# Kernel optimization log

Measured on AMD Instinct MI355X. Metric: run time of the kernel, lower is better.

## Reference

```python
import jax, jax.numpy as jnp
import numpy as np

B, T, I, H, O, L = 128, 512, 64, 256, 2, 2


def _gru_layer(x_seq, w_ih, w_hh, b_ih, b_hh):
    # x_seq: [B, T, in], w_ih: [3H, in], w_hh: [3H, H], biases: [3H]
    # PyTorch gate order: r, z, n
    xg = jnp.einsum('bti,gi->btg', x_seq, w_ih) + b_ih  # [B, T, 3H]
    h0 = jnp.zeros((x_seq.shape[0], w_hh.shape[1]), x_seq.dtype)

    def step(h, xg_t):
        hg = h @ w_hh.T + b_hh  # [B, 3H]
        xr, xz, xn = jnp.split(xg_t, 3, axis=-1)
        hr, hz, hn = jnp.split(hg, 3, axis=-1)
        r = jax.nn.sigmoid(xr + hr)
        z = jax.nn.sigmoid(xz + hz)
        n = jnp.tanh(xn + r * hn)
        h_new = (1.0 - z) * n + z * h
        return h_new, h_new

    _, hs = jax.lax.scan(step, h0, jnp.swapaxes(xg, 0, 1))  # [T, B, H]
    return jnp.swapaxes(hs, 0, 1)  # [B, T, H]


def setup_inputs() -> dict:
    key = jax.random.key(0)
    ks = jax.random.split(key, 12)
    s_ih0 = 1.0 / np.sqrt(H)
    inp = {
        'x': jax.random.normal(ks[0], (B, T, I), jnp.float32),
        'w_ih0': jax.random.uniform(ks[1], (3 * H, I), jnp.float32, -s_ih0, s_ih0),
        'w_hh0': jax.random.uniform(ks[2], (3 * H, H), jnp.float32, -s_ih0, s_ih0),
        'b_ih0': jax.random.uniform(ks[3], (3 * H,), jnp.float32, -s_ih0, s_ih0),
        'b_hh0': jax.random.uniform(ks[4], (3 * H,), jnp.float32, -s_ih0, s_ih0),
        'w_ih1': jax.random.uniform(ks[5], (3 * H, H), jnp.float32, -s_ih0, s_ih0),
        'w_hh1': jax.random.uniform(ks[6], (3 * H, H), jnp.float32, -s_ih0, s_ih0),
        'b_ih1': jax.random.uniform(ks[7], (3 * H,), jnp.float32, -s_ih0, s_ih0),
        'b_hh1': jax.random.uniform(ks[8], (3 * H,), jnp.float32, -s_ih0, s_ih0),
        'fc_w': jax.random.uniform(ks[9], (O, H), jnp.float32, -s_ih0, s_ih0),
        'fc_b': jax.random.uniform(ks[10], (O,), jnp.float32, -s_ih0, s_ih0),
    }
    return inp


def reference(x, w_ih0, w_hh0, b_ih0, b_hh0, w_ih1, w_hh1, b_ih1, b_hh1, fc_w, fc_b):
    h1 = _gru_layer(x, w_ih0, w_hh0, b_ih0, b_hh0)   # [B, T, H]
    h2 = _gru_layer(h1, w_ih1, w_hh1, b_ih1, b_hh1)  # [B, T, H]
    last = jax.nn.relu(h2[:, -1])                     # [B, H]
    return last @ fc_w.T + fc_b                       # [B, O]
```

## Files before the change

### kernel.cpp

```cpp
#include <hip/hip_runtime.h>


namespace {
constexpr int kB = 128, kT = 512, kI = 64, kH = 256, kBH = kB * kH;
constexpr int RPG = 16, NWG = 256, NT = 512;

constexpr int SRS = 36;
constexpr int SKS = 16 * SRS + 4;
constexpr int O_S0 = 0;
constexpr int O_S1 = O_S0 + 8 * SKS;
constexpr int O_X  = O_S1 + 8 * SKS;
constexpr int O_PB = O_X + RPG * 68;
constexpr int PBN  = 4 * 16 * 36;
constexpr int LDSF = O_PB + PBN;
}

using ull = unsigned long long;
using u32 = unsigned;

__device__ __forceinline__ float sigf(float v) { return 1.0f / (1.0f + expf(-v)); }
__device__ __forceinline__ float dot4(const float4 a, const float4 b) {
  return a.x * b.x + a.y * b.y + a.z * b.z + a.w * b.w;
}
__device__ __forceinline__ float red8(float v) {
  v += __shfl_xor(v, 8);
  v += __shfl_xor(v, 16);
  v += __shfl_xor(v, 32);
  return v;
}
#define F4(p) (*(const float4*)(p))
#define AL(p)    __hip_atomic_load((p), __ATOMIC_RELAXED, __HIP_MEMORY_SCOPE_AGENT)
#define AS(p, v) __hip_atomic_store((p), (v), __ATOMIC_RELAXED, __HIP_MEMORY_SCOPE_AGENT)

__global__ __launch_bounds__(NT, 2) void gru_persistent(
    const float* __restrict__ x,
    const float* __restrict__ wih0, const float* __restrict__ whh0,
    const float* __restrict__ bih0, const float* __restrict__ bhh0,
    const float* __restrict__ wih1, const float* __restrict__ whh1,
    const float* __restrict__ bih1, const float* __restrict__ bhh1,
    const float* __restrict__ fcw, const float* __restrict__ fcb,
    u32* __restrict__ h0w,
    u32* __restrict__ h1w,
    float* __restrict__ out)
{
  __shared__ float lds[2 * LDSF];

  const int bid = blockIdx.x;
  const int g   = bid >> 5;
  const int wg  = bid & 31;
  const int tid = threadIdx.x;
  const int r0  = g * RPG;
  const int j0  = wg * 8;

  const int wave = tid >> 6, lane = tid & 63;
  const int lay  = wave >> 2;
  const int fam  = (wave >> 1) & 1;
  const int rh   = wave & 1;
  const int ju   = lane & 7;
  const int ks   = lane >> 3;
  const int jg   = j0 + ju;

  for (int i = tid; i < PBN; i += NT) {
    lds[O_PB + i] = 0.f;
    lds[LDSF + O_PB + i] = 0.f;
  }

  float4 wr0[8], wr1[8], wr2[8];
  if (lay == 0) {
    if (fam == 0) {
#define L0F0(wrg, gg) { \
      const float* wi = wih0 + (size_t)((gg) * kH + jg) * kI + ks * 8;   \
      const float* wh = whh0 + (size_t)((gg) * kH + jg) * kH + ks * 32;  \
      wrg[0] = F4(wi); wrg[1] = F4(wi + 4);                              \
      wrg[2] = F4(wh); wrg[3] = F4(wh + 4); wrg[4] = F4(wh + 8); }
      L0F0(wr0, 0) L0F0(wr1, 1) L0F0(wr2, 2)
    } else {
#define L0F1(wrg, gg) { \
      const float* wh = whh0 + (size_t)((gg) * kH + jg) * kH + ks * 32 + 12; \
      wrg[0] = F4(wh); wrg[1] = F4(wh + 4); wrg[2] = F4(wh + 8);             \
      wrg[3] = F4(wh + 12); wrg[4] = F4(wh + 16); }
      L0F1(wr0, 0) L0F1(wr1, 1) L0F1(wr2, 2)
    }
  } else {
    const float* ws = fam ? whh1 : wih1;
#define L1W(wrg, gg) { \
    const float* wp = ws + (size_t)((gg) * kH + jg) * kH + ks * 32;          \
    wrg[0] = F4(wp);      wrg[1] = F4(wp + 4);  wrg[2] = F4(wp + 8);         \
    wrg[3] = F4(wp + 12); wrg[4] = F4(wp + 16); wrg[5] = F4(wp + 20);        \
    wrg[6] = F4(wp + 24); wrg[7] = F4(wp + 28); }
    L1W(wr0, 0) L1W(wr1, 1) L1W(wr2, 2)
  }

  float fb_r = 0.f, fb_z = 0.f, fn_i = 0.f, fn_h = 0.f;
  if (tid < 256) {
    const int layf = tid >> 7, uf = tid & 7, jf = j0 + uf;
    const float* bi = layf ? bih1 : bih0;
    const float* bh = layf ? bhh1 : bhh0;
    fb_r = bi[jf] + bh[jf];
    fb_z = bi[kH + jf] + bh[kH + jf];
    fn_i = bi[2 * kH + jf];
    fn_h = bh[2 * kH + jf];
  }

  int RO[4], K2[4];
  #pragma unroll
  for (int p = 0; p < 4; ++p) {
    const int i = tid + p * NT;
    RO[p] = i >> 7; K2[p] = i & 127;
  }

  auto finish_u = [&](int u, const float* Lp) {
    if (tid < 256) {
      const int layf = tid >> 7;
      const bool act = layf ? (u >= 1) : (u < kT);
      if (act) {
        const int rof = (tid >> 3) & 15, uf = tid & 7, jf = j0 + uf;
        const float* p0 = Lp + O_PB + ((layf * 2) * 16 + rof) * SRS + uf;
        const float* p1 = p0 + 16 * SRS;
        const float rr = sigf(p0[0] + p1[0] + fb_r);
        const float zz = sigf(p0[8] + p1[8] + fb_z);
        const float nn = tanhf(p0[16] + p1[16] + fn_i +
                               rr * (p0[24] + p1[24] + fn_h));
        const float hp = Lp[(layf ? O_S1 : O_S0) +
                            (jf >> 5) * SKS + rof * SRS + (jf & 31)];
        const float hv = (1.f - zz) * nn + zz * hp;
        const int slot = layf ? ((u - 1) % 3) : (u % 3);
        const u32 tag = layf ? (u32)(u & 3) : (u32)((u + 1) & 3);
        const u32 bits = (__float_as_uint(hv) & ~3u) | tag;
        u32* hw = (layf ? h1w : h0w) + (size_t)slot * kBH +
                  (size_t)(r0 + rof) * kH + jf;
        AS(hw, bits);
      }
    }
  };

  __syncthreads();

  for (int s = 0; s <= kT; ++s) {
    float* Lc = lds + (s & 1) * LDSF;
    const float* Lp = lds + ((s & 1) ^ 1) * LDSF;

    const int slot0 = (s + 2) % 3;
    const int slot1 = (s + 1) % 3;
    const u32 e0 = (u32)(s & 3);
    const u32 e1 = (u32)((s - 1) & 3);

    const ull* A0[4]; const ull* A1[4];
    ull v0[4], v1[4];
    #pragma unroll
    for (int p = 0; p < 4; ++p) {
      A0[p] = (const ull*)(h0w + (size_t)slot0 * kBH +
                           (size_t)(r0 + RO[p]) * kH) + K2[p];
      v0[p] = AL(A0[p]);
    }
    if (s >= 1) {
      #pragma unroll
      for (int p = 0; p < 4; ++p) {
        A1[p] = (const ull*)(h1w + (size_t)slot1 * kBH +
                             (size_t)(r0 + RO[p]) * kH) + K2[p];
        v1[p] = AL(A1[p]);
      }
    }
    float4 xv = {};
    if (s < kT && tid < 256) {
      const int ro = tid >> 4, c4 = (tid & 15) * 4;
      xv = F4(x + (size_t)(r0 + ro) * kT * kI + (size_t)s * kI + c4);
    }

    if (s >= 1) finish_u(s - 1, Lp);
    asm volatile("" ::: "memory");

    for (;;) {
      u32 bad = 0;
      #pragma unroll
      for (int p = 0; p < 4; ++p)
        bad |= ((u32)v0[p] ^ e0) | ((u32)(v0[p] >> 32) ^ e0);
      if (s >= 1) {
        #pragma unroll
        for (int p = 0; p < 4; ++p)
          bad |= ((u32)v1[p] ^ e1) | ((u32)(v1[p] >> 32) ^ e1);
      }
      if (!(bad & 3u)) break;
      __builtin_amdgcn_s_sleep(1);
      #pragma unroll
      for (int p = 0; p < 4; ++p) v0[p] = AL(A0[p]);
      if (s >= 1) {
        #pragma unroll
        for (int p = 0; p < 4; ++p) v1[p] = AL(A1[p]);
      }
    }
    #pragma unroll
    for (int p = 0; p < 4; ++p) {
      const int ksg = K2[p] >> 4, off = (K2[p] * 2) & 31, ro = RO[p];
      float2 f0; __builtin_memcpy(&f0, &v0[p], 8);
      *(float2*)(Lc + O_S0 + ksg * SKS + ro * SRS + off) = f0;
      if (s >= 1) {
        float2 f1; __builtin_memcpy(&f1, &v1[p], 8);
        *(float2*)(Lc + O_S1 + ksg * SKS + ro * SRS + off) = f1;
      }
    }
    if (s < kT && tid < 256) {
      const int ro = tid >> 4, c4 = (tid & 15) * 4;
      *(float4*)(Lc + O_X + ro * 68 + c4) = xv;
    }
    __syncthreads();

    const bool wact = lay ? (s >= 1) : (s < kT);
    if (wact) {
      float prr[8], pzz[8], pni[8], pnh[8];
      #pragma unroll
      for (int r = 0; r < 8; ++r) {
        const int ro = rh * 8 + r;
        float pr = 0.f, pz = 0.f, pxi = 0.f, pxh = 0.f;
        if (lay == 0) {
          if (fam == 0) {
            const float* ax = Lc + O_X + ro * 68 + ks * 8;
            const float4 x0 = F4(ax), x1 = F4(ax + 4);
            pr  += dot4(x0, wr0[0]) + dot4(x1, wr0[1]);
            pz  += dot4(x0, wr1[0]) + dot4(x1, wr1[1]);
            pxi += dot4(x0, wr2[0]) + dot4(x1, wr2[1]);
            const float* ah = Lc + O_S0 + ks * SKS + ro * SRS;
            #pragma unroll
            for (int i = 0; i < 3; ++i) {
              const float4 hv = F4(ah + i * 4);
              pr  += dot4(hv, wr0[2 + i]);
              pz  += dot4(hv, wr1[2 + i]);
              pxh += dot4(hv, wr2[2 + i]);
            }
          } else {
            const float* ah = Lc + O_S0 + ks * SKS + ro * SRS + 12;
            #pragma unroll
            for (int i = 0; i < 5; ++i) {
              const float4 hv = F4(ah + i * 4);
              pr  += dot4(hv, wr0[i]);
              pz  += dot4(hv, wr1[i]);
              pxh += dot4(hv, wr2[i]);
            }
          }
        } else {
          const float* aa = Lc + (fam ? O_S1 : O_S0) + ks * SKS + ro * SRS;
          #pragma unroll
          for (int i = 0; i < 8; ++i) {
            const float4 av = F4(aa + i * 4);
            pr += dot4(av, wr0[i]);
            pz += dot4(av, wr1[i]);
            if (fam) pxh += dot4(av, wr2[i]);
            else     pxi += dot4(av, wr2[i]);
          }
        }
        prr[r] = pr; pzz[r] = pz; pni[r] = pxi; pnh[r] = pxh;
      }
      #pragma unroll
      for (int r = 0; r < 8; ++r) { prr[r] = red8(prr[r]); pzz[r] = red8(pzz[r]); }
      if (lay == 0 && fam == 0) {
        #pragma unroll
        for (int r = 0; r < 8; ++r) { pni[r] = red8(pni[r]); pnh[r] = red8(pnh[r]); }
      } else if (fam == 0) {
        #pragma unroll
        for (int r = 0; r < 8; ++r) pni[r] = red8(pni[r]);
      } else {
        #pragma unroll
        for (int r = 0; r < 8; ++r) pnh[r] = red8(pnh[r]);
      }
      if (ks == 0) {
        #pragma unroll
        for (int r = 0; r < 8; ++r) {
          float* pb = Lc + O_PB + ((wave >> 1) * 16 + rh * 8 + r) * SRS + ju;
          pb[0] = prr[r]; pb[8] = pzz[r];
          if (lay == 0 && fam == 0) { pb[16] = pni[r]; pb[24] = pnh[r]; }
          else if (fam == 0)          pb[16] = pni[r];
          else                        pb[24] = pnh[r];
        }
      }
    }
    __syncthreads();
  }

  finish_u(kT, lds + (kT & 1) * LDSF);

  if (wg == 0 && tid < 256) {
    const int rv = tid >> 4, o = (tid >> 3) & 1, kseg = tid & 7;
    const u32* hf = h1w + (size_t)((kT - 1) % 3) * kBH + (size_t)(r0 + rv) * kH;
    const float* wfc = fcw + (size_t)o * kH;
    float acc = 0.f;
    for (int k = kseg * 32; k < kseg * 32 + 32; ++k) {
      u32 b;
      do {
        b = AL(hf + k);
      } while ((b & 3u) != (u32)(kT & 3));
      acc += fmaxf(__uint_as_float(b), 0.f) * wfc[k];
    }
    acc += __shfl_xor(acc, 1);
    acc += __shfl_xor(acc, 2);
    acc += __shfl_xor(acc, 4);
    if (kseg == 0) out[(r0 + rv) * 2 + o] = acc + fcb[o];
  }
}

extern "C" void kernel_launch(void* const* d_in, const int* in_sizes, int n_in,
                              void* d_out, int out_size, void* d_ws, size_t ws_size,
                              hipStream_t stream) {
  const float* x    = (const float*)d_in[0];
  const float* wih0 = (const float*)d_in[1];
  const float* whh0 = (const float*)d_in[2];
  const float* bih0 = (const float*)d_in[3];
  const float* bhh0 = (const float*)d_in[4];
  const float* wih1 = (const float*)d_in[5];
  const float* whh1 = (const float*)d_in[6];
  const float* bih1 = (const float*)d_in[7];
  const float* bhh1 = (const float*)d_in[8];
  const float* fcw  = (const float*)d_in[9];
  const float* fcb  = (const float*)d_in[10];

  u32* h0w = (u32*)d_ws;
  u32* h1w = h0w + 3 * kBH;
  float* out = (float*)d_out;

  hipMemsetAsync(d_ws, 0, (size_t)(6 * kBH) * sizeof(u32), stream);

  gru_persistent<<<NWG, NT, 0, stream>>>(
      x, wih0, whh0, bih0, bhh0, wih1, whh1, bih1, bhh1,
      fcw, fcb, h0w, h1w, out);
}
```

Before: 4.083 ms.

## Stagger layer-0 and layer-1 phases within each step using single-buffered LDS

```diff
diff --git a/kernel.cpp b/kernel.cpp
--- a/kernel.cpp
+++ b/kernel.cpp
@@ -43,7 +43,7 @@
     u32* __restrict__ h1w,
     float* __restrict__ out)
 {
-  __shared__ float lds[2 * LDSF];
+  __shared__ float lds[LDSF];
 
   const int bid = blockIdx.x;
   const int g   = bid >> 5;
@@ -60,10 +60,7 @@
   const int ks   = lane >> 3;
   const int jg   = j0 + ju;
 
-  for (int i = tid; i < PBN; i += NT) {
-    lds[O_PB + i] = 0.f;
-    lds[LDSF + O_PB + i] = 0.f;
-  }
+  for (int i = tid; i < PBN; i += NT) lds[O_PB + i] = 0.f;
 
   float4 wr0[8], wr1[8], wr2[8];
   if (lay == 0) {
@@ -92,134 +89,65 @@
   }
 
   float fb_r = 0.f, fb_z = 0.f, fn_i = 0.f, fn_h = 0.f;
+  if (tid < 128) {
+    const int jf = j0 + (tid & 7);
+    fb_r = bih0[jf] + bhh0[jf];
+    fb_z = bih0[kH + jf] + bhh0[kH + jf];
+    fn_i = bih0[2 * kH + jf];
+    fn_h = bhh0[2 * kH + jf];
+  } else if (tid >= 256 && tid < 384) {
+    const int jf = j0 + (tid & 7);
+    fb_r = bih1[jf] + bhh1[jf];
+    fb_z = bih1[kH + jf] + bhh1[kH + jf];
+    fn_i = bih1[2 * kH + jf];
+    fn_h = bhh1[2 * kH + jf];
+  }
+
+  const int sidx = tid & 255;
+  int RO[8], K2[8];
+  #pragma unroll
+  for (int p = 0; p < 8; ++p) {
+    const int i = sidx + p * 256;
+    RO[p] = i >> 7; K2[p] = i & 127;
+  }
+
   if (tid < 256) {
-    const int layf = tid >> 7, uf = tid & 7, jf = j0 + uf;
-    const float* bi = layf ? bih1 : bih0;
-    const float* bh = layf ? bhh1 : bhh0;
-    fb_r = bi[jf] + bh[jf];
-    fb_z = bi[kH + jf] + bh[kH + jf];
-    fn_i = bi[2 * kH + jf];
-    fn_h = bh[2 * kH + jf];
-  }
-
-  int RO[4], K2[4];
-  #pragma unroll
-  for (int p = 0; p < 4; ++p) {
-    const int i = tid + p * NT;
-    RO[p] = i >> 7; K2[p] = i & 127;
-  }
-
-  auto finish_u = [&](int u, const float* Lp) {
-    if (tid < 256) {
-      const int layf = tid >> 7;
-      const bool act = layf ? (u >= 1) : (u < kT);
-      if (act) {
-        const int rof = (tid >> 3) & 15, uf = tid & 7, jf = j0 + uf;
-        const float* p0 = Lp + O_PB + ((layf * 2) * 16 + rof) * SRS + uf;
-        const float* p1 = p0 + 16 * SRS;
-        const float rr = sigf(p0[0] + p1[0] + fb_r);
-        const float zz = sigf(p0[8] + p1[8] + fb_z);
-        const float nn = tanhf(p0[16] + p1[16] + fn_i +
-                               rr * (p0[24] + p1[24] + fn_h));
-        const float hp = Lp[(layf ? O_S1 : O_S0) +
-                            (jf >> 5) * SKS + rof * SRS + (jf & 31)];
-        const float hv = (1.f - zz) * nn + zz * hp;
-        const int slot = layf ? ((u - 1) % 3) : (u % 3);
-        const u32 tag = layf ? (u32)(u & 3) : (u32)((u + 1) & 3);
-        const u32 bits = (__float_as_uint(hv) & ~3u) | tag;
-        u32* hw = (layf ? h1w : h0w) + (size_t)slot * kBH +
-                  (size_t)(r0 + rof) * kH + jf;
-        AS(hw, bits);
-      }
-    }
-  };
-
+    #pragma unroll
+    for (int p = 0; p < 8; ++p) {
+      const ull* a0 = (const ull*)(h0w + (size_t)2 * kBH +
+                                   (size_t)(r0 + RO[p]) * kH) + K2[p];
+      ull v = AL(a0);
+      while ((((u32)v | (u32)(v >> 32)) & 3u)) {
+        __builtin_amdgcn_s_sleep(1);
+        v = AL(a0);
+      }
+      const int ksg = K2[p] >> 4, off = (K2[p] * 2) & 31;
+      float2 f; __builtin_memcpy(&f, &v, 8);
+      *(float2*)(lds + O_S0 + ksg * SKS + RO[p] * SRS + off) = f;
+    }
+  } else {
+    const int idx = tid - 256;
+    const int ro = idx >> 4, c4 = (idx & 15) * 4;
+    *(float4*)(lds + O_X + ro * 68 + c4) =
+        F4(x + (size_t)(r0 + ro) * kT * kI + c4);
+  }
   __syncthreads();
 
   for (int s = 0; s <= kT; ++s) {
-    float* Lc = lds + (s & 1) * LDSF;
-    const float* Lp = lds + ((s & 1) ^ 1) * LDSF;
-
-    const int slot0 = (s + 2) % 3;
-    const int slot1 = (s + 1) % 3;
-    const u32 e0 = (u32)(s & 3);
-    const u32 e1 = (u32)((s - 1) & 3);
-
-    const ull* A0[4]; const ull* A1[4];
-    ull v0[4], v1[4];
-    #pragma unroll
-    for (int p = 0; p < 4; ++p) {
-      A0[p] = (const ull*)(h0w + (size_t)slot0 * kBH +
-                           (size_t)(r0 + RO[p]) * kH) + K2[p];
-      v0[p] = AL(A0[p]);
-    }
-    if (s >= 1) {
-      #pragma unroll
-      for (int p = 0; p < 4; ++p) {
-        A1[p] = (const ull*)(h1w + (size_t)slot1 * kBH +
-                             (size_t)(r0 + RO[p]) * kH) + K2[p];
-        v1[p] = AL(A1[p]);
-      }
-    }
-    float4 xv = {};
-    if (s < kT && tid < 256) {
-      const int ro = tid >> 4, c4 = (tid & 15) * 4;
-      xv = F4(x + (size_t)(r0 + ro) * kT * kI + (size_t)s * kI + c4);
-    }
-
-    if (s >= 1) finish_u(s - 1, Lp);
-    asm volatile("" ::: "memory");
-
-    for (;;) {
-      u32 bad = 0;
-      #pragma unroll
-      for (int p = 0; p < 4; ++p)
-        bad |= ((u32)v0[p] ^ e0) | ((u32)(v0[p] >> 32) ^ e0);
-      if (s >= 1) {
-        #pragma unroll
-        for (int p = 0; p < 4; ++p)
-          bad |= ((u32)v1[p] ^ e1) | ((u32)(v1[p] >> 32) ^ e1);
-      }
-      if (!(bad & 3u)) break;
-      __builtin_amdgcn_s_sleep(1);
-      #pragma unroll
-      for (int p = 0; p < 4; ++p) v0[p] = AL(A0[p]);
-      if (s >= 1) {
-        #pragma unroll
-        for (int p = 0; p < 4; ++p) v1[p] = AL(A1[p]);
-      }
-    }
-    #pragma unroll
-    for (int p = 0; p < 4; ++p) {
-      const int ksg = K2[p] >> 4, off = (K2[p] * 2) & 31, ro = RO[p];
-      float2 f0; __builtin_memcpy(&f0, &v0[p], 8);
-      *(float2*)(Lc + O_S0 + ksg * SKS + ro * SRS + off) = f0;
-      if (s >= 1) {
-        float2 f1; __builtin_memcpy(&f1, &v1[p], 8);
-        *(float2*)(Lc + O_S1 + ksg * SKS + ro * SRS + off) = f1;
-      }
-    }
-    if (s < kT && tid < 256) {
-      const int ro = tid >> 4, c4 = (tid & 15) * 4;
-      *(float4*)(Lc + O_X + ro * 68 + c4) = xv;
-    }
-    __syncthreads();
-
-    const bool wact = lay ? (s >= 1) : (s < kT);
-    if (wact) {
-      float prr[8], pzz[8], pni[8], pnh[8];
-      #pragma unroll
-      for (int r = 0; r < 8; ++r) {
-        const int ro = rh * 8 + r;
-        float pr = 0.f, pz = 0.f, pxi = 0.f, pxh = 0.f;
-        if (lay == 0) {
+    if (lay == 0) {
+      if (s < kT) {
+        float prr[8], pzz[8], pni[8], pnh[8];
+        #pragma unroll
+        for (int r = 0; r < 8; ++r) {
+          const int ro = rh * 8 + r;
+          float pr = 0.f, pz = 0.f, pxi = 0.f, pxh = 0.f;
           if (fam == 0) {
-            const float* ax = Lc + O_X + ro * 68 + ks * 8;
+            const float* ax = lds + O_X + ro * 68 + ks * 8;
             const float4 x0 = F4(ax), x1 = F4(ax + 4);
             pr  += dot4(x0, wr0[0]) + dot4(x1, wr0[1]);
             pz  += dot4(x0, wr1[0]) + dot4(x1, wr1[1]);
             pxi += dot4(x0, wr2[0]) + dot4(x1, wr2[1]);
-            const float* ah = Lc + O_S0 + ks * SKS + ro * SRS;
+            const float* ah = lds + O_S0 + ks * SKS + ro * SRS;
             #pragma unroll
             for (int i = 0; i < 3; ++i) {
               const float4 hv = F4(ah + i * 4);
@@ -228,7 +156,7 @@
               pxh += dot4(hv, wr2[2 + i]);
             }
           } else {
-            const float* ah = Lc + O_S0 + ks * SKS + ro * SRS + 12;
+            const float* ah = lds + O_S0 + ks * SKS + ro * SRS + 12;
             #pragma unroll
             for (int i = 0; i < 5; ++i) {
               const float4 hv = F4(ah + i * 4);
@@ -237,8 +165,92 @@
               pxh += dot4(hv, wr2[i]);
             }
           }
+          prr[r] = pr; pzz[r] = pz; pni[r] = pxi; pnh[r] = pxh;
+        }
+        #pragma unroll
+        for (int r = 0; r < 8; ++r) { prr[r] = red8(prr[r]); pzz[r] = red8(pzz[r]); }
+        if (fam == 0) {
+          #pragma unroll
+          for (int r = 0; r < 8; ++r) { pni[r] = red8(pni[r]); pnh[r] = red8(pnh[r]); }
         } else {
-          const float* aa = Lc + (fam ? O_S1 : O_S0) + ks * SKS + ro * SRS;
+          #pragma unroll
+          for (int r = 0; r < 8; ++r) pnh[r] = red8(pnh[r]);
+        }
+        if (ks == 0) {
+          #pragma unroll
+          for (int r = 0; r < 8; ++r) {
+            float* pb = lds + O_PB + ((wave >> 1) * 16 + rh * 8 + r) * SRS + ju;
+            pb[0] = prr[r]; pb[8] = pzz[r];
+            if (fam == 0) { pb[16] = pni[r]; pb[24] = pnh[r]; }
+            else            pb[24] = pnh[r];
+          }
+        }
+      }
+    } else {
+      if (s >= 1) {
+        const int slot1 = (s + 1) % 3;
+        const u32 e1 = (u32)((s - 1) & 3);
+        const ull* A1[8]; ull v1[8];
+        #pragma unroll
+        for (int p = 0; p < 8; ++p) {
+          A1[p] = (const ull*)(h1w + (size_t)slot1 * kBH +
+                               (size_t)(r0 + RO[p]) * kH) + K2[p];
+          v1[p] = AL(A1[p]);
+        }
+        for (;;) {
+          u32 bad = 0;
+          #pragma unroll
+          for (int p = 0; p < 8; ++p)
+            bad |= ((u32)v1[p] ^ e1) | ((u32)(v1[p] >> 32) ^ e1);
+          if (!(bad & 3u)) break;
+          __builtin_amdgcn_s_sleep(1);
+          #pragma unroll
+          for (int p = 0; p < 8; ++p) v1[p] = AL(A1[p]);
+        }
+        #pragma unroll
+        for (int p = 0; p < 8; ++p) {
+          const int ksg = K2[p] >> 4, off = (K2[p] * 2) & 31;
+          float2 f; __builtin_memcpy(&f, &v1[p], 8);
+          *(float2*)(lds + O_S1 + ksg * SKS + RO[p] * SRS + off) = f;
+        }
+      }
+    }
+    __syncthreads();
+
+    if (tid < 128) {
+      if (s < kT) {
+        const int rof = tid >> 3, uf = tid & 7, jf = j0 + uf;
+        const float* p0 = lds + O_PB + (0 * 16 + rof) * SRS + uf;
+        const float* p1 = p0 + 16 * SRS;
+        const float rr = sigf(p0[0] + p1[0] + fb_r);
+        const float zz = sigf(p0[8] + p1[8] + fb_z);
+        const float nn = tanhf(p0[16] + p1[16] + fn_i +
+                               rr * (p0[24] + p1[24] + fn_h));
+        const float hp = lds[O_S0 + (jf >> 5) * SKS + rof * SRS + (jf & 31)];
+        const float hv = (1.f - zz) * nn + zz * hp;
+        const u32 bits = (__float_as_uint(hv) & ~3u) | (u32)((s + 1) & 3);
+        AS(h0w + (size_t)(s % 3) * kBH + (size_t)(r0 + rof) * kH + jf, bits);
+      }
+    } else if (tid < 256) {
+      if (s + 1 < kT) {
+        const int t = tid - 128;
+        #pragma unroll
+        for (int qq = 0; qq < 2; ++qq) {
+          const int idx = t + qq * 128;
+          const int ro = idx >> 4, c4 = (idx & 15) * 4;
+          *(float4*)(lds + O_X + ro * 68 + c4) =
+              F4(x + (size_t)(r0 + ro) * kT * kI + (size_t)(s + 1) * kI + c4);
+        }
+      }
+    } else {
+      if (s >= 1) {
+        const float* base = lds + (fam ? O_S1 : O_S0);
+        float prr[8], pzz[8], pni[8], pnh[8];
+        #pragma unroll
+        for (int r = 0; r < 8; ++r) {
+          const int ro = rh * 8 + r;
+          float pr = 0.f, pz = 0.f, pxi = 0.f, pxh = 0.f;
+          const float* aa = base + ks * SKS + ro * SRS;
           #pragma unroll
           for (int i = 0; i < 8; ++i) {
             const float4 av = F4(aa + i * 4);
@@ -247,36 +259,76 @@
             if (fam) pxh += dot4(av, wr2[i]);
             else     pxi += dot4(av, wr2[i]);
           }
-        }
-        prr[r] = pr; pzz[r] = pz; pni[r] = pxi; pnh[r] = pxh;
-      }
-      #pragma unroll
-      for (int r = 0; r < 8; ++r) { prr[r] = red8(prr[r]); pzz[r] = red8(pzz[r]); }
-      if (lay == 0 && fam == 0) {
-        #pragma unroll
-        for (int r = 0; r < 8; ++r) { pni[r] = red8(pni[r]); pnh[r] = red8(pnh[r]); }
-      } else if (fam == 0) {
-        #pragma unroll
-        for (int r = 0; r < 8; ++r) pni[r] = red8(pni[r]);
-      } else {
-        #pragma unroll
-        for (int r = 0; r < 8; ++r) pnh[r] = red8(pnh[r]);
-      }
-      if (ks == 0) {
-        #pragma unroll
-        for (int r = 0; r < 8; ++r) {
-          float* pb = Lc + O_PB + ((wave >> 1) * 16 + rh * 8 + r) * SRS + ju;
-          pb[0] = prr[r]; pb[8] = pzz[r];
-          if (lay == 0 && fam == 0) { pb[16] = pni[r]; pb[24] = pnh[r]; }
-          else if (fam == 0)          pb[16] = pni[r];
-          else                        pb[24] = pnh[r];
+          prr[r] = pr; pzz[r] = pz; pni[r] = pxi; pnh[r] = pxh;
+        }
+        #pragma unroll
+        for (int r = 0; r < 8; ++r) { prr[r] = red8(prr[r]); pzz[r] = red8(pzz[r]); }
+        if (fam == 0) {
+          #pragma unroll
+          for (int r = 0; r < 8; ++r) pni[r] = red8(pni[r]);
+        } else {
+          #pragma unroll
+          for (int r = 0; r < 8; ++r) pnh[r] = red8(pnh[r]);
+        }
+        if (ks == 0) {
+          #pragma unroll
+          for (int r = 0; r < 8; ++r) {
+            float* pb = lds + O_PB + ((wave >> 1) * 16 + rh * 8 + r) * SRS + ju;
+            pb[0] = prr[r]; pb[8] = pzz[r];
+            if (fam == 0) pb[16] = pni[r];
+            else          pb[24] = pnh[r];
+          }
         }
       }
     }
     __syncthreads();
-  }
-
-  finish_u(kT, lds + (kT & 1) * LDSF);
+
+    if (tid >= 256 && tid < 384) {
+      if (s >= 1) {
+        const int t = tid - 256;
+        const int rof = t >> 3, uf = t & 7, jf = j0 + uf;
+        const float* p0 = lds + O_PB + (2 * 16 + rof) * SRS + uf;
+        const float* p1 = p0 + 16 * SRS;
+        const float rr = sigf(p0[0] + p1[0] + fb_r);
+        const float zz = sigf(p0[8] + p1[8] + fb_z);
+        const float nn = tanhf(p0[16] + p1[16] + fn_i +
+                               rr * (p0[24] + p1[24] + fn_h));
+        const float hp = lds[O_S1 + (jf >> 5) * SKS + rof * SRS + (jf & 31)];
+        const float hv = (1.f - zz) * nn + zz * hp;
+        const u32 bits = (__float_as_uint(hv) & ~3u) | (u32)(s & 3);
+        AS(h1w + (size_t)((s - 1) % 3) * kBH + (size_t)(r0 + rof) * kH + jf, bits);
+      }
+    } else if (tid < 256) {
+      if (s < kT) {
+        const int slot0 = s % 3;
+        const u32 e0 = (u32)((s + 1) & 3);
+        const ull* A0[8]; ull v0[8];
+        #pragma unroll
+        for (int p = 0; p < 8; ++p) {
+          A0[p] = (const ull*)(h0w + (size_t)slot0 * kBH +
+                               (size_t)(r0 + RO[p]) * kH) + K2[p];
+          v0[p] = AL(A0[p]);
+        }
+        for (;;) {
+          u32 bad = 0;
+          #pragma unroll
+          for (int p = 0; p < 8; ++p)
+            bad |= ((u32)v0[p] ^ e0) | ((u32)(v0[p] >> 32) ^ e0);
+          if (!(bad & 3u)) break;
+          __builtin_amdgcn_s_sleep(1);
+          #pragma unroll
+          for (int p = 0; p < 8; ++p) v0[p] = AL(A0[p]);
+        }
+        #pragma unroll
+        for (int p = 0; p < 8; ++p) {
+          const int ksg = K2[p] >> 4, off = (K2[p] * 2) & 31;
+          float2 f; __builtin_memcpy(&f, &v0[p], 8);
+          *(float2*)(lds + O_S0 + ksg * SKS + RO[p] * SRS + off) = f;
+        }
+      }
+    }
+    __syncthreads();
+  }
 
   if (wg == 0 && tid < 256) {
     const int rv = tid >> 4, o = (tid >> 3) & 1, kseg = tid & 7;
```

After: 5.578 ms. +36.6%, slower.

## Halve rows per workgroup to 8 and finish gates in-step with single LDS buffer

Applied to the files above, without the earlier changes.

```diff
diff --git a/kernel.cpp b/kernel.cpp
--- a/kernel.cpp
+++ b/kernel.cpp
@@ -3,15 +3,15 @@
 
 namespace {
 constexpr int kB = 128, kT = 512, kI = 64, kH = 256, kBH = kB * kH;
-constexpr int RPG = 16, NWG = 256, NT = 512;
+constexpr int RPG = 8, NWG = 512, NT = 512;
 
 constexpr int SRS = 36;
-constexpr int SKS = 16 * SRS + 4;
+constexpr int SKS = 8 * SRS + 4;
 constexpr int O_S0 = 0;
 constexpr int O_S1 = O_S0 + 8 * SKS;
 constexpr int O_X  = O_S1 + 8 * SKS;
 constexpr int O_PB = O_X + RPG * 68;
-constexpr int PBN  = 4 * 16 * 36;
+constexpr int PBN  = 4 * 8 * 36;
 constexpr int LDSF = O_PB + PBN;
 }
 
@@ -32,7 +32,7 @@
 #define AL(p)    __hip_atomic_load((p), __ATOMIC_RELAXED, __HIP_MEMORY_SCOPE_AGENT)
 #define AS(p, v) __hip_atomic_store((p), (v), __ATOMIC_RELAXED, __HIP_MEMORY_SCOPE_AGENT)
 
-__global__ __launch_bounds__(NT, 2) void gru_persistent(
+__global__ __launch_bounds__(NT, 4) void gru_persistent(
     const float* __restrict__ x,
     const float* __restrict__ wih0, const float* __restrict__ whh0,
     const float* __restrict__ bih0, const float* __restrict__ bhh0,
@@ -43,7 +43,7 @@
     u32* __restrict__ h1w,
     float* __restrict__ out)
 {
-  __shared__ float lds[2 * LDSF];
+  __shared__ float lds[LDSF];
 
   const int bid = blockIdx.x;
   const int g   = bid >> 5;
@@ -60,10 +60,7 @@
   const int ks   = lane >> 3;
   const int jg   = j0 + ju;
 
-  for (int i = tid; i < PBN; i += NT) {
-    lds[O_PB + i] = 0.f;
-    lds[LDSF + O_PB + i] = 0.f;
-  }
+  for (int i = tid; i < PBN; i += NT) lds[O_PB + i] = 0.f;
 
   float4 wr0[8], wr1[8], wr2[8];
   if (lay == 0) {
@@ -92,8 +89,8 @@
   }
 
   float fb_r = 0.f, fb_z = 0.f, fn_i = 0.f, fn_h = 0.f;
-  if (tid < 256) {
-    const int layf = tid >> 7, uf = tid & 7, jf = j0 + uf;
+  if (tid < 128) {
+    const int layf = tid >> 6, uf = tid & 7, jf = j0 + uf;
     const float* bi = layf ? bih1 : bih0;
     const float* bh = layf ? bhh1 : bhh0;
     fb_r = bi[jf] + bh[jf];
@@ -102,124 +99,78 @@
     fn_h = bh[2 * kH + jf];
   }
 
-  int RO[4], K2[4];
-  #pragma unroll
-  for (int p = 0; p < 4; ++p) {
-    const int i = tid + p * NT;
-    RO[p] = i >> 7; K2[p] = i & 127;
-  }
-
-  auto finish_u = [&](int u, const float* Lp) {
-    if (tid < 256) {
-      const int layf = tid >> 7;
-      const bool act = layf ? (u >= 1) : (u < kT);
-      if (act) {
-        const int rof = (tid >> 3) & 15, uf = tid & 7, jf = j0 + uf;
-        const float* p0 = Lp + O_PB + ((layf * 2) * 16 + rof) * SRS + uf;
-        const float* p1 = p0 + 16 * SRS;
-        const float rr = sigf(p0[0] + p1[0] + fb_r);
-        const float zz = sigf(p0[8] + p1[8] + fb_z);
-        const float nn = tanhf(p0[16] + p1[16] + fn_i +
-                               rr * (p0[24] + p1[24] + fn_h));
-        const float hp = Lp[(layf ? O_S1 : O_S0) +
-                            (jf >> 5) * SKS + rof * SRS + (jf & 31)];
-        const float hv = (1.f - zz) * nn + zz * hp;
-        const int slot = layf ? ((u - 1) % 3) : (u % 3);
-        const u32 tag = layf ? (u32)(u & 3) : (u32)((u + 1) & 3);
-        const u32 bits = (__float_as_uint(hv) & ~3u) | tag;
-        u32* hw = (layf ? h1w : h0w) + (size_t)slot * kBH +
-                  (size_t)(r0 + rof) * kH + jf;
-        AS(hw, bits);
-      }
-    }
-  };
+  const int SRO = tid >> 6;
+  const int SK2 = (2 * tid) & 127;
 
   __syncthreads();
 
   for (int s = 0; s <= kT; ++s) {
-    float* Lc = lds + (s & 1) * LDSF;
-    const float* Lp = lds + ((s & 1) ^ 1) * LDSF;
-
     const int slot0 = (s + 2) % 3;
     const int slot1 = (s + 1) % 3;
     const u32 e0 = (u32)(s & 3);
     const u32 e1 = (u32)((s - 1) & 3);
 
-    const ull* A0[4]; const ull* A1[4];
-    ull v0[4], v1[4];
-    #pragma unroll
-    for (int p = 0; p < 4; ++p) {
-      A0[p] = (const ull*)(h0w + (size_t)slot0 * kBH +
-                           (size_t)(r0 + RO[p]) * kH) + K2[p];
-      v0[p] = AL(A0[p]);
-    }
-    if (s >= 1) {
-      #pragma unroll
-      for (int p = 0; p < 4; ++p) {
-        A1[p] = (const ull*)(h1w + (size_t)slot1 * kBH +
-                             (size_t)(r0 + RO[p]) * kH) + K2[p];
-        v1[p] = AL(A1[p]);
-      }
-    }
     float4 xv = {};
-    if (s < kT && tid < 256) {
+    if (s < kT && tid < 128) {
       const int ro = tid >> 4, c4 = (tid & 15) * 4;
       xv = F4(x + (size_t)(r0 + ro) * kT * kI + (size_t)s * kI + c4);
     }
 
-    if (s >= 1) finish_u(s - 1, Lp);
-    asm volatile("" ::: "memory");
-
+    const ull* A0 = (const ull*)(h0w + (size_t)slot0 * kBH +
+                                 (size_t)(r0 + SRO) * kH) + SK2;
+    ull v00 = AL(A0), v01 = AL(A0 + 1);
+    const ull* A1 = nullptr;
+    ull v10 = 0, v11 = 0;
+    if (s >= 1) {
+      A1 = (const ull*)(h1w + (size_t)slot1 * kBH +
+                        (size_t)(r0 + SRO) * kH) + SK2;
+      v10 = AL(A1); v11 = AL(A1 + 1);
+    }
     for (;;) {
-      u32 bad = 0;
-      #pragma unroll
-      for (int p = 0; p < 4; ++p)
-        bad |= ((u32)v0[p] ^ e0) | ((u32)(v0[p] >> 32) ^ e0);
-      if (s >= 1) {
-        #pragma unroll
-        for (int p = 0; p < 4; ++p)
-          bad |= ((u32)v1[p] ^ e1) | ((u32)(v1[p] >> 32) ^ e1);
-      }
+      u32 bad = ((u32)v00 ^ e0) | ((u32)(v00 >> 32) ^ e0) |
+                ((u32)v01 ^ e0) | ((u32)(v01 >> 32) ^ e0);
+      if (s >= 1)
+        bad |= ((u32)v10 ^ e1) | ((u32)(v10 >> 32) ^ e1) |
+               ((u32)v11 ^ e1) | ((u32)(v11 >> 32) ^ e1);
       if (!(bad & 3u)) break;
       __builtin_amdgcn_s_sleep(1);
-      #pragma unroll
-      for (int p = 0; p < 4; ++p) v0[p] = AL(A0[p]);
+      v00 = AL(A0); v01 = AL(A0 + 1);
+      if (s >= 1) { v10 = AL(A1); v11 = AL(A1 + 1); }
+    }
+    {
+      const int ksg = SK2 >> 4, off = (SK2 * 2) & 31;
+      float4 f0;
+      f0.x = __uint_as_float((u32)v00); f0.y = __uint_as_float((u32)(v00 >> 32));
+      f0.z = __uint_as_float((u32)v01); f0.w = __uint_as_float((u32)(v01 >> 32));
+      *(float4*)(lds + O_S0 + ksg * SKS + SRO * SRS + off) = f0;
       if (s >= 1) {
-        #pragma unroll
-        for (int p = 0; p < 4; ++p) v1[p] = AL(A1[p]);
-      }
-    }
-    #pragma unroll
-    for (int p = 0; p < 4; ++p) {
-      const int ksg = K2[p] >> 4, off = (K2[p] * 2) & 31, ro = RO[p];
-      float2 f0; __builtin_memcpy(&f0, &v0[p], 8);
-      *(float2*)(Lc + O_S0 + ksg * SKS + ro * SRS + off) = f0;
-      if (s >= 1) {
-        float2 f1; __builtin_memcpy(&f1, &v1[p], 8);
-        *(float2*)(Lc + O_S1 + ksg * SKS + ro * SRS + off) = f1;
-      }
-    }
-    if (s < kT && tid < 256) {
+        float4 f1;
+        f1.x = __uint_as_float((u32)v10); f1.y = __uint_as_float((u32)(v10 >> 32));
+        f1.z = __uint_as_float((u32)v11); f1.w = __uint_as_float((u32)(v11 >> 32));
+        *(float4*)(lds + O_S1 + ksg * SKS + SRO * SRS + off) = f1;
+      }
+    }
+    if (s < kT && tid < 128) {
       const int ro = tid >> 4, c4 = (tid & 15) * 4;
-      *(float4*)(Lc + O_X + ro * 68 + c4) = xv;
+      *(float4*)(lds + O_X + ro * 68 + c4) = xv;
     }
     __syncthreads();
 
     const bool wact = lay ? (s >= 1) : (s < kT);
     if (wact) {
-      float prr[8], pzz[8], pni[8], pnh[8];
+      float prr[4], pzz[4], pni[4], pnh[4];
       #pragma unroll
-      for (int r = 0; r < 8; ++r) {
-        const int ro = rh * 8 + r;
+      for (int r = 0; r < 4; ++r) {
+        const int ro = rh * 4 + r;
         float pr = 0.f, pz = 0.f, pxi = 0.f, pxh = 0.f;
         if (lay == 0) {
           if (fam == 0) {
-            const float* ax = Lc + O_X + ro * 68 + ks * 8;
+            const float* ax = lds + O_X + ro * 68 + ks * 8;
             const float4 x0 = F4(ax), x1 = F4(ax + 4);
             pr  += dot4(x0, wr0[0]) + dot4(x1, wr0[1]);
             pz  += dot4(x0, wr1[0]) + dot4(x1, wr1[1]);
             pxi += dot4(x0, wr2[0]) + dot4(x1, wr2[1]);
-            const float* ah = Lc + O_S0 + ks * SKS + ro * SRS;
+            const float* ah = lds + O_S0 + ks * SKS + ro * SRS;
             #pragma unroll
             for (int i = 0; i < 3; ++i) {
               const float4 hv = F4(ah + i * 4);
@@ -228,7 +179,7 @@
               pxh += dot4(hv, wr2[2 + i]);
             }
           } else {
-            const float* ah = Lc + O_S0 + ks * SKS + ro * SRS + 12;
+            const float* ah = lds + O_S0 + ks * SKS + ro * SRS + 12;
             #pragma unroll
             for (int i = 0; i < 5; ++i) {
               const float4 hv = F4(ah + i * 4);
@@ -238,7 +189,7 @@
             }
           }
         } else {
-          const float* aa = Lc + (fam ? O_S1 : O_S0) + ks * SKS + ro * SRS;
+          const float* aa = lds + (fam ? O_S1 : O_S0) + ks * SKS + ro * SRS;
           #pragma unroll
           for (int i = 0; i < 8; ++i) {
             const float4 av = F4(aa + i * 4);
@@ -251,21 +202,22 @@
         prr[r] = pr; pzz[r] = pz; pni[r] = pxi; pnh[r] = pxh;
       }
       #pragma unroll
-      for (int r = 0; r < 8; ++r) { prr[r] = red8(prr[r]); pzz[r] = red8(pzz[r]); }
+      for (int r = 0; r < 4; ++r) { prr[r] = red8(prr[r]); pzz[r] = red8(pzz[r]); }
       if (lay == 0 && fam == 0) {
         #pragma unroll
-        for (int r = 0; r < 8; ++r) { pni[r] = red8(pni[r]); pnh[r] = red8(pnh[r]); }
+        for (int r = 0; r < 4; ++r) { pni[r] = red8(pni[r]); pnh[r] = red8(pnh[r]); }
       } else if (fam == 0) {
         #pragma unroll
-        for (int r = 0; r < 8; ++r) pni[r] = red8(pni[r]);
+        for (int r = 0; r < 4; ++r) pni[r] = red8(pni[r]);
       } else {
         #pragma unroll
-        for (int r = 0; r < 8; ++r) pnh[r] = red8(pnh[r]);
+        for (int r = 0; r < 4; ++r) pnh[r] = red8(pnh[r]);
       }
       if (ks == 0) {
         #pragma unroll
-        for (int r = 0; r < 8; ++r) {
-          float* pb = Lc + O_PB + ((wave >> 1) * 16 + rh * 8 + r) * SRS + ju;
+        for (int r = 0; r < 4; ++r) {
+          const int ro = rh * 4 + r;
+          float* pb = lds + O_PB + ((wave >> 1) * 8 + ro) * SRS + ju;
           pb[0] = prr[r]; pb[8] = pzz[r];
           if (lay == 0 && fam == 0) { pb[16] = pni[r]; pb[24] = pnh[r]; }
           else if (fam == 0)          pb[16] = pni[r];
@@ -274,11 +226,34 @@
       }
     }
     __syncthreads();
-  }
-
-  finish_u(kT, lds + (kT & 1) * LDSF);
-
-  if (wg == 0 && tid < 256) {
+
+    if (tid < 128) {
+      const int layf = tid >> 6;
+      const bool act = layf ? (s >= 1) : (s < kT);
+      if (act) {
+        const int local = tid & 63, rof = local >> 3, uf = local & 7;
+        const int jf = j0 + uf;
+        const float* p0 = lds + O_PB + ((layf * 2) * 8 + rof) * SRS + uf;
+        const float* p1 = p0 + 8 * SRS;
+        const float rr = sigf(p0[0] + p1[0] + fb_r);
+        const float zz = sigf(p0[8] + p1[8] + fb_z);
+        const float nn = tanhf(p0[16] + p1[16] + fn_i +
+                               rr * (p0[24] + p1[24] + fn_h));
+        const float hp = lds[(layf ? O_S1 : O_S0) +
+                             (jf >> 5) * SKS + rof * SRS + (jf & 31)];
+        const float hv = (1.f - zz) * nn + zz * hp;
+        const int slot = layf ? ((s - 1) % 3) : (s % 3);
+        const u32 tag = layf ? (u32)(s & 3) : (u32)((s + 1) & 3);
+        const u32 bits = (__float_as_uint(hv) & ~3u) | tag;
+        u32* hw = (layf ? h1w : h0w) + (size_t)slot * kBH +
+                  (size_t)(r0 + rof) * kH + jf;
+        AS(hw, bits);
+      }
+    }
+    __syncthreads();
+  }
+
+  if (wg == 0 && tid < 128) {
     const int rv = tid >> 4, o = (tid >> 3) & 1, kseg = tid & 7;
     const u32* hf = h1w + (size_t)((kT - 1) % 3) * kBH + (size_t)(r0 + rv) * kH;
     const float* wfc = fcw + (size_t)o * kH;
```

Result: slower. 9.809 ms (+140.2%).
